# Kernel optimization log

Measured on AMD Instinct MI355X. Metric: run time of the kernel, lower is better.

Reference implementation:

```python
import jax, jax.numpy as jnp
import numpy as np

B, S, EMBED, DK, DV, M = 8, 1024, 1024, 512, 512, 64


def setup_inputs() -> dict:
    key = jax.random.key(0)
    ks = jax.random.split(key, 9)
    query_in = jax.random.normal(ks[0], (B, S, EMBED), dtype=jnp.float32)
    key_in = jax.random.normal(ks[1], (B, S, EMBED), dtype=jnp.float32)
    value_in = jax.random.normal(ks[2], (B, S, EMBED), dtype=jnp.float32)
    lim = 1.0 / np.sqrt(EMBED)  # nn.Linear default init range
    u = lambda k, shape: jax.random.uniform(k, shape, minval=-lim, maxval=lim, dtype=jnp.float32)
    return {
        'query_in': query_in, 'key_in': key_in, 'value_in': value_in,
        'Wq': u(ks[3], (DK, EMBED)), 'bq': u(ks[4], (DK,)),
        'Wk': u(ks[5], (DK, EMBED)), 'bk': u(ks[6], (DK,)),
        'Wv': u(ks[7], (DV, EMBED)), 'bv': u(ks[8], (DV,)),
    }


def _select_landmarks(k_proj, m):
    # Original code runs recursive RLS sampling (random, host-side) over the m
    # segment-rows of key.reshape(B, m, seg, d) and gathers m of them back,
    # then flattens to (B, S, d). We use a deterministic data-dependent
    # selection (rows ranked by squared norm) with identical gather structure.
    Bb, Ss, d = k_proj.shape
    seg = Ss // m
    kr = k_proj.reshape(Bb, m, seg, d)
    scores = jnp.sum(kr * kr, axis=(2, 3))                      # [B, m]
    idx = jnp.argsort(-scores, axis=1)                          # [B, m]
    land = jnp.take_along_axis(kr, idx[:, :, None, None], axis=1)
    return land.reshape(Bb, Ss, d)                              # [B, S, d]


def reference(query_in, key_in, value_in, Wq, bq, Wk, bk, Wv, bv):
    scaling = DK ** -0.25  # 1/sqrt(sqrt(d_k)), applied to both q and k
    q = (jnp.einsum('bse,de->bsd', query_in, Wq) + bq) * scaling
    k = (jnp.einsum('bse,de->bsd', key_in, Wk) + bk) * scaling
    v = jnp.einsum('bse,de->bsd', value_in, Wv) + bv

    kl = _select_landmarks(k, M)                                # [B, S, DK]
    # is_decoder_self_attn is hard-coded True upstream -> q_landmarks = q,
    # so kernel_2 == kernel_1.
    kernel_1 = jax.nn.softmax(jnp.einsum('bqd,bkd->bqk', q, kl), axis=-1)
    kernel_2 = kernel_1
    kernel_3 = jax.nn.softmax(jnp.einsum('bqd,bkd->bqk', q, k), axis=-1)

    k2_inv = jnp.linalg.pinv(kernel_2)                          # [B, S, S] batched SVD
    out = jnp.einsum('bqk,bkd->bqd', jnp.einsum('bqm,bmk->bqk', kernel_1, k2_inv),
                     jnp.einsum('bqk,bkd->bqd', kernel_3, v))
    # dropout is identity in eval mode
    return out
```

## Files before the change

kernel.cpp:

```cpp
#include <hip/hip_runtime.h>
#include <hip/hip_bf16.h>

#define SS   1024
#define DKK  512

typedef __hip_bfloat16 bf16;
typedef __attribute__((ext_vector_type(8))) short s16x8;
typedef __attribute__((ext_vector_type(8))) unsigned short u16x8;
typedef __attribute__((ext_vector_type(4))) float f32x4;

#define WS_W(z)  ((48ull << 20) + ((size_t)(z) << 20))
#define WS_ST    (51ull << 20)
#define WS_Q     (52ull << 20)
#define WS_K     (60ull << 20)
#define WS_VT    (68ull << 20)
#define WS_LG    (0ull)

__device__ __forceinline__ void async_ld16(const void* g, void* s) {
  __builtin_amdgcn_global_load_lds(
      (const __attribute__((address_space(1))) void*)g,
      (__attribute__((address_space(3))) void*)s, 16, 0, 0);
}

__device__ __forceinline__ unsigned short f2bfu(float f) {
  return __builtin_bit_cast(unsigned short, __float2bfloat16(f));
}
__device__ __forceinline__ float bfu2f(unsigned short u) {
  unsigned int i = ((unsigned int)u) << 16;
  return __builtin_bit_cast(float, i);
}

__global__ __launch_bounds__(256)
void convert_w(const float* __restrict__ w0, const float* __restrict__ w1,
               const float* __restrict__ w2, char* __restrict__ ws)
{
  const int bx = blockIdx.x;
  const int z = bx >> 8, local = bx & 255;
  const float* src = (z == 0) ? w0 : (z == 1) ? w1 : w2;
  unsigned short* dst = (unsigned short*)(ws + WS_W(z));
  const int i = local * 2048 + threadIdx.x * 8;
  const float4* s = (const float4*)(src + i);
  float4 a = s[0], b = s[1];
  ushort4 o0, o1;
  o0.x = f2bfu(a.x); o0.y = f2bfu(a.y); o0.z = f2bfu(a.z); o0.w = f2bfu(a.w);
  o1.x = f2bfu(b.x); o1.y = f2bfu(b.y); o1.z = f2bfu(b.z); o1.w = f2bfu(b.w);
  ((ushort4*)(dst + i))[0] = o0;
  ((ushort4*)(dst + i))[1] = o1;
}

template<int BM, int BN, int K, int LDA, int LDB>
__device__ __forceinline__ void gemm_core(const bf16* __restrict__ A,
                                          const bf16* __restrict__ Bw,
                                          int bm, int bn,
                                          short* As, short* Bs, f32x4* acc)
{
  constexpr int MI = BM / 32, NI = BN / 32;
  constexpr int AR = BM / 4,  BR = BN / 4;
  const int tid  = threadIdx.x;
  const int lane = tid & 63;
  const int wave = tid >> 6;
  const int l8   = lane >> 3;
  const int kch  = ((lane & 7) ^ l8) * 8;
  const bf16* ag = A  + (size_t)(bm * BM + wave * AR + l8) * LDA + kch;
  const bf16* bg = Bw + (size_t)(bn * BN + wave * BR + l8) * LDB + kch;
  short* AsW = As + wave * AR * 64;
  short* BsW = Bs + wave * BR * 64;
  const int waveM = wave >> 1, waveN = wave & 1;
  const int l16  = lane & 15;
  const int quad = lane >> 4;
  const int xr   = l16 & 7;

  #pragma unroll
  for (int t = 0; t < MI * NI; ++t)
    #pragma unroll
    for (int r = 0; r < 4; ++r) acc[t][r] = 0.0f;

  for (int kt = 0; kt < K / 64; ++kt) {
    #pragma unroll
    for (int j = 0; j < AR / 8; ++j) async_ld16(ag + (size_t)j * 8 * LDA, AsW + j * 8 * 64);
    #pragma unroll
    for (int j = 0; j < BR / 8; ++j) async_ld16(bg + (size_t)j * 8 * LDB, BsW + j * 8 * 64);
    ag += 64; bg += 64;
    __syncthreads();
    #pragma unroll
    for (int ks = 0; ks < 2; ++ks) {
      s16x8 af[MI], bfv[NI];
      #pragma unroll
      for (int mi = 0; mi < MI; ++mi) {
        const int row  = waveM * (BM / 2) + mi * 16 + l16;
        const int slot = (ks * 4 + quad) ^ xr;
        af[mi] = *(const s16x8*)&As[row * 64 + slot * 8];
      }
      #pragma unroll
      for (int ni = 0; ni < NI; ++ni) {
        const int row  = waveN * (BN / 2) + ni * 16 + l16;
        const int slot = (ks * 4 + quad) ^ xr;
        bfv[ni] = *(const s16x8*)&Bs[row * 64 + slot * 8];
      }
      #pragma unroll
      for (int mi = 0; mi < MI; ++mi)
        #pragma unroll
        for (int ni = 0; ni < NI; ++ni)
          acc[mi * NI + ni] = __builtin_amdgcn_mfma_f32_16x16x32_bf16(
              af[mi], bfv[ni], acc[mi * NI + ni], 0, 0, 0);
    }
    __syncthreads();
  }
}

template<int K, int LDA, int LDB>
__device__ __forceinline__ void gemm_core_f32a(const float* __restrict__ A,
                                               const bf16* __restrict__ Bw,
                                               int bm, int bn,
                                               short* As, short* Bs, f32x4* acc)
{
  const int tid  = threadIdx.x;
  const int lane = tid & 63;
  const int wave = tid >> 6;
  const int l8   = lane >> 3;
  const int kch  = ((lane & 7) ^ l8) * 8;
  const bf16* bg = Bw + (size_t)(bn * 256 + wave * 64 + l8) * LDB + kch;
  short* BsW = Bs + wave * 64 * 64;
  const int arow = tid >> 3;
  const int ag8  = tid & 7;
  const int slotA = (ag8 ^ (arow & 7)) * 8;
  const float* ag = A + (size_t)(bm * 64 + arow) * LDA + ag8 * 8;
  const int waveM = wave >> 1, waveN = wave & 1;
  const int l16  = lane & 15;
  const int quad = lane >> 4;
  const int xr   = l16 & 7;

  #pragma unroll
  for (int t = 0; t < 16; ++t)
    #pragma unroll
    for (int r = 0; r < 4; ++r) acc[t][r] = 0.0f;

  for (int kt = 0; kt < K / 64; ++kt) {
    #pragma unroll
    for (int j = 0; j < 8; ++j) async_ld16(bg + (size_t)j * 8 * LDB, BsW + j * 8 * 64);
    bg += 64;
    #pragma unroll
    for (int p = 0; p < 2; ++p) {
      const float4* s = (const float4*)(ag + (size_t)p * 32 * LDA);
      float4 a = s[0], b = s[1];
      u16x8 v;
      v[0] = f2bfu(a.x); v[1] = f2bfu(a.y); v[2] = f2bfu(a.z); v[3] = f2bfu(a.w);
      v[4] = f2bfu(b.x); v[5] = f2bfu(b.y); v[6] = f2bfu(b.z); v[7] = f2bfu(b.w);
      *(u16x8*)&As[(p * 32 + arow) * 64 + slotA] = v;
    }
    ag += 64;
    __syncthreads();
    #pragma unroll
    for (int ks = 0; ks < 2; ++ks) {
      s16x8 af[2], bfv[8];
      #pragma unroll
      for (int mi = 0; mi < 2; ++mi) {
        const int row  = waveM * 32 + mi * 16 + l16;
        const int slot = (ks * 4 + quad) ^ xr;
        af[mi] = *(const s16x8*)&As[row * 64 + slot * 8];
      }
      #pragma unroll
      for (int ni = 0; ni < 8; ++ni) {
        const int row  = waveN * 128 + ni * 16 + l16;
        const int slot = (ks * 4 + quad) ^ xr;
        bfv[ni] = *(const s16x8*)&Bs[row * 64 + slot * 8];
      }
      #pragma unroll
      for (int mi = 0; mi < 2; ++mi)
        #pragma unroll
        for (int ni = 0; ni < 8; ++ni)
          acc[mi * 8 + ni] = __builtin_amdgcn_mfma_f32_16x16x32_bf16(
              af[mi], bfv[ni], acc[mi * 8 + ni], 0, 0, 0);
    }
    __syncthreads();
  }
}

__global__ __launch_bounds__(256, 3)
void proj_kernel(const float* __restrict__ Xq, const float* __restrict__ Xk,
                 const float* __restrict__ Xv, const bf16* __restrict__ W0,
                 const float* __restrict__ bq, const float* __restrict__ bk,
                 const float* __restrict__ bv,
                 bf16* __restrict__ qo, bf16* __restrict__ ko,
                 bf16* __restrict__ vT, float qscale)
{
  __shared__ __align__(16) short As[64 * 64];
  __shared__ __align__(16) short Bs[256 * 64];
  const int id   = blockIdx.x;
  const int xcd  = id & 7;
  const int s    = id >> 3;
  const int bn   = s & 1;
  const int pair = (s >> 1) * 8 + xcd;
  const int bm   = pair & 127;
  const int z    = pair >> 7;
  const float* A  = (z == 0) ? Xq : (z == 1) ? Xk : Xv;
  const bf16*  Bw = W0 + ((size_t)z << 19);
  const float* bias = (z == 0) ? bq : (z == 1) ? bk : bv;
  f32x4 acc[16];
  gemm_core_f32a<1024, 1024, 1024>(A, Bw, bm, bn, As, Bs, acc);

  const int lane = threadIdx.x & 63;
  const int wave = threadIdx.x >> 6;
  const int waveM = wave >> 1, waveN = wave & 1;
  const int l16 = lane & 15, quad = lane >> 4;
  const int row0 = bm * 64 + waveM * 32;
  const int col0 = bn * 256 + waveN * 128;
  const float sc = (z == 0) ? qscale : 1.0f;
  bf16* C = (z == 0) ? qo : ko;
  #pragma unroll
  for (int ni = 0; ni < 8; ++ni) {
    const int col = col0 + ni * 16 + l16;
    const float bb = bias[col];
    #pragma unroll
    for (int mi = 0; mi < 2; ++mi)
      #pragma unroll
      for (int r = 0; r < 4; ++r) {
        const int row = row0 + mi * 16 + quad * 4 + r;
        const float v = acc[mi * 8 + ni][r] + bb;
        if (z == 2)
          vT[((size_t)(row >> 10) * DKK + col) * SS + (row & (SS - 1))] =
              __float2bfloat16(v);
        else
          C[(size_t)row * DKK + col] = __float2bfloat16(v * sc);
      }
  }
}

__global__ __launch_bounds__(256, 3)
void scores_kernel(const bf16* __restrict__ q, const bf16* __restrict__ k,
                   unsigned short* __restrict__ Pp, float* __restrict__ stats)
{
  __shared__ __align__(16) short As[128 * 64];
  __shared__ __align__(16) short Bs[128 * 64];
  const int z = blockIdx.z;
  const int bn = blockIdx.x, bm = blockIdx.y;
  f32x4 acc[16];
  gemm_core<128, 128, 512, 512, 512>(q + (size_t)z * SS * DKK,
                                     k + (size_t)z * SS * DKK,
                                     bm, bn, As, Bs, acc);

  const int lane = threadIdx.x & 63;
  const int wave = threadIdx.x >> 6;
  const int waveM = wave >> 1, waveN = wave & 1;
  const int l16 = lane & 15, quad = lane >> 4;
  const int row0 = bm * 128 + waveM * 64;
  const int col0 = bn * 128 + waveN * 64;
  const int chunk = bn * 2 + waveN;
  unsigned short* C = Pp + (size_t)z * SS * SS;
  #pragma unroll
  for (int mi = 0; mi < 4; ++mi)
    #pragma unroll
    for (int r = 0; r < 4; ++r) {
      const int row = row0 + mi * 16 + quad * 4 + r;
      float x[4];
      #pragma unroll
      for (int ni = 0; ni < 4; ++ni) x[ni] = acc[mi * 4 + ni][r];
      float m = fmaxf(fmaxf(x[0], x[1]), fmaxf(x[2], x[3]));
      #pragma unroll
      for (int msk = 1; msk < 16; msk <<= 1) m = fmaxf(m, __shfl_xor(m, msk));
      float e[4], ssum = 0.f;
      #pragma unroll
      for (int ni = 0; ni < 4; ++ni) { e[ni] = __expf(x[ni] - m); ssum += e[ni]; }
      #pragma unroll
      for (int msk = 1; msk < 16; msk <<= 1) ssum += __shfl_xor(ssum, msk);
      #pragma unroll
      for (int ni = 0; ni < 4; ++ni)
        C[(size_t)row * SS + col0 + ni * 16 + l16] = f2bfu(e[ni]);
      if (l16 == 0) {
        float2 mr; mr.x = m; mr.y = ssum;
        *(float2*)&stats[(((size_t)z * SS + row) * 16 + chunk) * 2] = mr;
      }
    }
}

__device__ __forceinline__ void gemm_core_pvF(const unsigned short* __restrict__ Pp,
                                              const bf16* __restrict__ vT,
                                              int bm, int bn, const float* Fl,
                                              short* As, short* Bs, f32x4* acc)
{
  const int tid  = threadIdx.x;
  const int lane = tid & 63;
  const int wave = tid >> 6;
  const int l8   = lane >> 3;
  const int kch  = ((lane & 7) ^ l8) * 8;
  const bf16* bg = vT + (size_t)(bn * 64 + wave * 16 + l8) * 1024 + kch;
  short* BsW = Bs + wave * 16 * 64;
  const int arow = tid >> 3;
  const int ag8  = tid & 7;
  const int slotA = (ag8 ^ (arow & 7)) * 8;
  const unsigned short* ag = Pp + (size_t)(bm * 128 + arow) * 1024 + ag8 * 8;
  const int waveM = wave >> 1, waveN = wave & 1;
  const int l16  = lane & 15;
  const int quad = lane >> 4;
  const int xr   = l16 & 7;

  #pragma unroll
  for (int t = 0; t < 8; ++t)
    #pragma unroll
    for (int r = 0; r < 4; ++r) acc[t][r] = 0.0f;

  for (int kt = 0; kt < 16; ++kt) {
    #pragma unroll
    for (int j = 0; j < 2; ++j) async_ld16(bg + (size_t)j * 8 * 1024, BsW + j * 8 * 64);
    bg += 64;
    #pragma unroll
    for (int p = 0; p < 4; ++p) {
      const int rl = p * 32 + arow;
      u16x8 u = *(const u16x8*)(ag + (size_t)p * 32 * 1024);
      const float f = Fl[rl * 17 + kt];
      u16x8 v;
      #pragma unroll
      for (int j = 0; j < 8; ++j)
        v[j] = f2bfu(bfu2f((unsigned short)u[j]) * f);
      *(u16x8*)&As[rl * 64 + slotA] = v;
    }
    ag += 64;
    __syncthreads();
    #pragma unroll
    for (int ks = 0; ks < 2; ++ks) {
      s16x8 af[4], bfv[2];
      #pragma unroll
      for (int mi = 0; mi < 4; ++mi) {
        const int row  = waveM * 64 + mi * 16 + l16;
        const int slot = (ks * 4 + quad) ^ xr;
        af[mi] = *(const s16x8*)&As[row * 64 + slot * 8];
      }
      #pragma unroll
      for (int ni = 0; ni < 2; ++ni) {
        const int row  = waveN * 32 + ni * 16 + l16;
        const int slot = (ks * 4 + quad) ^ xr;
        bfv[ni] = *(const s16x8*)&Bs[row * 64 + slot * 8];
      }
      #pragma unroll
      for (int mi = 0; mi < 4; ++mi)
        #pragma unroll
        for (int ni = 0; ni < 2; ++ni)
          acc[mi * 2 + ni] = __builtin_amdgcn_mfma_f32_16x16x32_bf16(
              af[mi], bfv[ni], acc[mi * 2 + ni], 0, 0, 0);
    }
    __syncthreads();
  }
}

__global__ __launch_bounds__(256, 3)
void pv_kernel(const unsigned short* __restrict__ Pp, const bf16* __restrict__ vT,
               const float* __restrict__ stats, float* __restrict__ out)
{
  __shared__ __align__(16) short As[128 * 64];
  __shared__ __align__(16) short Bs[64 * 64];
  __shared__ float Fl[128 * 17];
  const int z = blockIdx.z;
  const int bn = blockIdx.x, bm = blockIdx.y;
  const int tid = threadIdx.x;

  if (tid < 128) {
    const float* st = stats + ((size_t)z * SS + bm * 128 + tid) * 32;
    float mc[16], lc[16];
    float M = -1e30f;
    #pragma unroll
    for (int c = 0; c < 16; ++c) {
      mc[c] = st[c * 2]; lc[c] = st[c * 2 + 1];
      M = fmaxf(M, mc[c]);
    }
    float L = 0.f;
    #pragma unroll
    for (int c = 0; c < 16; ++c) {
      mc[c] = __expf(mc[c] - M);
      L += mc[c] * lc[c];
    }
    const float R = 1.0f / L;
    #pragma unroll
    for (int c = 0; c < 16; ++c) Fl[tid * 17 + c] = mc[c] * R;
  }
  __syncthreads();

  f32x4 acc[8];
  gemm_core_pvF(Pp + (size_t)z * SS * SS, vT + (size_t)z * DKK * SS,
                bm, bn, Fl, As, Bs, acc);

  const int lane = tid & 63;
  const int wave = tid >> 6;
  const int waveM = wave >> 1, waveN = wave & 1;
  const int l16 = lane & 15, quad = lane >> 4;
  const int row0 = bm * 128 + waveM * 64;
  const int col0 = bn * 64 + waveN * 32;
  float* C = out + (size_t)z * SS * DKK;
  #pragma unroll
  for (int ni = 0; ni < 2; ++ni) {
    const int col = col0 + ni * 16 + l16;
    #pragma unroll
    for (int mi = 0; mi < 4; ++mi)
      #pragma unroll
      for (int r = 0; r < 4; ++r) {
        const int row = row0 + mi * 16 + quad * 4 + r;
        C[(size_t)row * DKK + col] = acc[mi * 2 + ni][r];
      }
  }
}

extern "C" void kernel_launch(void* const* d_in, const int* in_sizes, int n_in,
                              void* d_out, int out_size, void* d_ws, size_t ws_size,
                              hipStream_t stream)
{
  char* ws = (char*)d_ws;
  bf16*  W0   = (bf16*)(ws + WS_W(0));
  float* stat = (float*)(ws + WS_ST);
  bf16*  q    = (bf16*)(ws + WS_Q);
  bf16*  kk   = (bf16*)(ws + WS_K);
  bf16*  vT   = (bf16*)(ws + WS_VT);
  unsigned short* Pp = (unsigned short*)(ws + WS_LG);

  const float qscale = 0.044194173824159216f;

  dim3 blk(256, 1, 1);
  hipLaunchKernelGGL(convert_w, dim3(768), blk, 0, stream,
                     (const float*)d_in[3], (const float*)d_in[5],
                     (const float*)d_in[7], ws);
  hipLaunchKernelGGL(proj_kernel, dim3(768, 1, 1), blk, 0, stream,
                     (const float*)d_in[0], (const float*)d_in[1],
                     (const float*)d_in[2], W0,
                     (const float*)d_in[4], (const float*)d_in[6],
                     (const float*)d_in[8], q, kk, vT, qscale);
  hipLaunchKernelGGL(scores_kernel, dim3(8, 8, 8), blk, 0, stream,
                     q, kk, Pp, stat);
  hipLaunchKernelGGL(pv_kernel, dim3(8, 8, 8), blk, 0, stream,
                     Pp, vT, stat, (float*)d_out);
}
```

Baseline: 221.8 us.

## Retile projection GEMM to 128x128 with async fp32 A staging in LDS

The projection kernel moves from 64x256 tiles to 128x128 tiles on a plain 3D grid, dropping the XCD-aware block remap. The fp32 activation tile is now copied straight into LDS with asynchronous global-to-LDS loads under an XOR swizzle, and the conversion to bf16 happens at fragment-read time instead of through registers before the store. This is meant to cut the register round-trip and the extra A-tile traffic and give a more balanced MFMA tile. In exchange it uses 48KB of LDS per block (fp32 A tile), which may lower occupancy, and each fragment is converted again whenever it is read.

```diff
diff --git a/kernel.cpp b/kernel.cpp
--- a/kernel.cpp
+++ b/kernel.cpp
@@ -108,74 +108,6 @@
   }
 }
 
-template<int K, int LDA, int LDB>
-__device__ __forceinline__ void gemm_core_f32a(const float* __restrict__ A,
-                                               const bf16* __restrict__ Bw,
-                                               int bm, int bn,
-                                               short* As, short* Bs, f32x4* acc)
-{
-  const int tid  = threadIdx.x;
-  const int lane = tid & 63;
-  const int wave = tid >> 6;
-  const int l8   = lane >> 3;
-  const int kch  = ((lane & 7) ^ l8) * 8;
-  const bf16* bg = Bw + (size_t)(bn * 256 + wave * 64 + l8) * LDB + kch;
-  short* BsW = Bs + wave * 64 * 64;
-  const int arow = tid >> 3;
-  const int ag8  = tid & 7;
-  const int slotA = (ag8 ^ (arow & 7)) * 8;
-  const float* ag = A + (size_t)(bm * 64 + arow) * LDA + ag8 * 8;
-  const int waveM = wave >> 1, waveN = wave & 1;
-  const int l16  = lane & 15;
-  const int quad = lane >> 4;
-  const int xr   = l16 & 7;
-
-  #pragma unroll
-  for (int t = 0; t < 16; ++t)
-    #pragma unroll
-    for (int r = 0; r < 4; ++r) acc[t][r] = 0.0f;
-
-  for (int kt = 0; kt < K / 64; ++kt) {
-    #pragma unroll
-    for (int j = 0; j < 8; ++j) async_ld16(bg + (size_t)j * 8 * LDB, BsW + j * 8 * 64);
-    bg += 64;
-    #pragma unroll
-    for (int p = 0; p < 2; ++p) {
-      const float4* s = (const float4*)(ag + (size_t)p * 32 * LDA);
-      float4 a = s[0], b = s[1];
-      u16x8 v;
-      v[0] = f2bfu(a.x); v[1] = f2bfu(a.y); v[2] = f2bfu(a.z); v[3] = f2bfu(a.w);
-      v[4] = f2bfu(b.x); v[5] = f2bfu(b.y); v[6] = f2bfu(b.z); v[7] = f2bfu(b.w);
-      *(u16x8*)&As[(p * 32 + arow) * 64 + slotA] = v;
-    }
-    ag += 64;
-    __syncthreads();
-    #pragma unroll
-    for (int ks = 0; ks < 2; ++ks) {
-      s16x8 af[2], bfv[8];
-      #pragma unroll
-      for (int mi = 0; mi < 2; ++mi) {
-        const int row  = waveM * 32 + mi * 16 + l16;
-        const int slot = (ks * 4 + quad) ^ xr;
-        af[mi] = *(const s16x8*)&As[row * 64 + slot * 8];
-      }
-      #pragma unroll
-      for (int ni = 0; ni < 8; ++ni) {
-        const int row  = waveN * 128 + ni * 16 + l16;
-        const int slot = (ks * 4 + quad) ^ xr;
-        bfv[ni] = *(const s16x8*)&Bs[row * 64 + slot * 8];
-      }
-      #pragma unroll
-      for (int mi = 0; mi < 2; ++mi)
-        #pragma unroll
-        for (int ni = 0; ni < 8; ++ni)
-          acc[mi * 8 + ni] = __builtin_amdgcn_mfma_f32_16x16x32_bf16(
-              af[mi], bfv[ni], acc[mi * 8 + ni], 0, 0, 0);
-    }
-    __syncthreads();
-  }
-}
-
 __global__ __launch_bounds__(256, 3)
 void proj_kernel(const float* __restrict__ Xq, const float* __restrict__ Xk,
                  const float* __restrict__ Xv, const bf16* __restrict__ W0,
@@ -184,39 +116,94 @@
                  bf16* __restrict__ qo, bf16* __restrict__ ko,
                  bf16* __restrict__ vT, float qscale)
 {
-  __shared__ __align__(16) short As[64 * 64];
-  __shared__ __align__(16) short Bs[256 * 64];
-  const int id   = blockIdx.x;
-  const int xcd  = id & 7;
-  const int s    = id >> 3;
-  const int bn   = s & 1;
-  const int pair = (s >> 1) * 8 + xcd;
-  const int bm   = pair & 127;
-  const int z    = pair >> 7;
+  __shared__ __align__(16) float Asf[128 * 64];
+  __shared__ __align__(16) short Bs[128 * 64];
+  const int z  = blockIdx.z;
+  const int bm = blockIdx.x, bn = blockIdx.y;
   const float* A  = (z == 0) ? Xq : (z == 1) ? Xk : Xv;
   const bf16*  Bw = W0 + ((size_t)z << 19);
   const float* bias = (z == 0) ? bq : (z == 1) ? bk : bv;
+
+  const int tid  = threadIdx.x;
+  const int lane = tid & 63;
+  const int wave = tid >> 6;
+  const int l8   = lane >> 3;
+  const int kchB = ((lane & 7) ^ l8) * 8;
+  const bf16* bg = Bw + (size_t)(bn * 128 + wave * 32 + l8) * 1024 + kchB;
+  short* BsW = Bs + wave * 32 * 64;
+  const int arow4 = lane >> 4;
+  const int aslot = lane & 15;
+  const float* ag_row = A + (size_t)(bm * 128 + wave * 32 + arow4) * 1024;
+  float* AsfW = Asf + (wave * 32) * 64;
+
+  const int waveM = wave >> 1, waveN = wave & 1;
+  const int l16  = lane & 15;
+  const int quad = lane >> 4;
+
   f32x4 acc[16];
-  gemm_core_f32a<1024, 1024, 1024>(A, Bw, bm, bn, As, Bs, acc);
-
-  const int lane = threadIdx.x & 63;
-  const int wave = threadIdx.x >> 6;
-  const int waveM = wave >> 1, waveN = wave & 1;
-  const int l16 = lane & 15, quad = lane >> 4;
-  const int row0 = bm * 64 + waveM * 32;
-  const int col0 = bn * 256 + waveN * 128;
+  #pragma unroll
+  for (int t = 0; t < 16; ++t)
+    #pragma unroll
+    for (int r = 0; r < 4; ++r) acc[t][r] = 0.0f;
+
+  for (int kt = 0; kt < 16; ++kt) {
+    #pragma unroll
+    for (int j = 0; j < 8; ++j) {
+      const int gch = aslot ^ ((j * 4 + arow4) & 15);
+      async_ld16(ag_row + (size_t)j * 4 * 1024 + kt * 64 + gch * 4,
+                 AsfW + j * 4 * 64);
+    }
+    #pragma unroll
+    for (int j = 0; j < 4; ++j)
+      async_ld16(bg + (size_t)j * 8 * 1024, BsW + j * 8 * 64);
+    bg += 64;
+    __syncthreads();
+    #pragma unroll
+    for (int ks = 0; ks < 2; ++ks) {
+      s16x8 af[4], bfv[4];
+      #pragma unroll
+      for (int mi = 0; mi < 4; ++mi) {
+        const int row = waveM * 64 + mi * 16 + l16;
+        const int c0  = ks * 8 + quad * 2;
+        const f32x4 a0 = *(const f32x4*)&Asf[row * 64 + ((c0 ^ l16) * 4)];
+        const f32x4 a1 = *(const f32x4*)&Asf[row * 64 + (((c0 + 1) ^ l16) * 4)];
+        u16x8 v;
+        v[0] = f2bfu(a0[0]); v[1] = f2bfu(a0[1]);
+        v[2] = f2bfu(a0[2]); v[3] = f2bfu(a0[3]);
+        v[4] = f2bfu(a1[0]); v[5] = f2bfu(a1[1]);
+        v[6] = f2bfu(a1[2]); v[7] = f2bfu(a1[3]);
+        af[mi] = __builtin_bit_cast(s16x8, v);
+      }
+      #pragma unroll
+      for (int ni = 0; ni < 4; ++ni) {
+        const int row  = waveN * 64 + ni * 16 + l16;
+        const int slot = (ks * 4 + quad) ^ (l16 & 7);
+        bfv[ni] = *(const s16x8*)&Bs[row * 64 + slot * 8];
+      }
+      #pragma unroll
+      for (int mi = 0; mi < 4; ++mi)
+        #pragma unroll
+        for (int ni = 0; ni < 4; ++ni)
+          acc[mi * 4 + ni] = __builtin_amdgcn_mfma_f32_16x16x32_bf16(
+              af[mi], bfv[ni], acc[mi * 4 + ni], 0, 0, 0);
+    }
+    __syncthreads();
+  }
+
+  const int row0 = bm * 128 + waveM * 64;
+  const int col0 = bn * 128 + waveN * 64;
   const float sc = (z == 0) ? qscale : 1.0f;
   bf16* C = (z == 0) ? qo : ko;
   #pragma unroll
-  for (int ni = 0; ni < 8; ++ni) {
+  for (int ni = 0; ni < 4; ++ni) {
     const int col = col0 + ni * 16 + l16;
     const float bb = bias[col];
     #pragma unroll
-    for (int mi = 0; mi < 2; ++mi)
+    for (int mi = 0; mi < 4; ++mi)
       #pragma unroll
       for (int r = 0; r < 4; ++r) {
         const int row = row0 + mi * 16 + quad * 4 + r;
-        const float v = acc[mi * 8 + ni][r] + bb;
+        const float v = acc[mi * 4 + ni][r] + bb;
         if (z == 2)
           vT[((size_t)(row >> 10) * DKK + col) * SS + (row & (SS - 1))] =
               __float2bfloat16(v);
@@ -416,7 +403,7 @@
   hipLaunchKernelGGL(convert_w, dim3(768), blk, 0, stream,
                      (const float*)d_in[3], (const float*)d_in[5],
                      (const float*)d_in[7], ws);
-  hipLaunchKernelGGL(proj_kernel, dim3(768, 1, 1), blk, 0, stream,
+  hipLaunchKernelGGL(proj_kernel, dim3(64, 4, 3), blk, 0, stream,
                      (const float*)d_in[0], (const float*)d_in[1],
                      (const float*)d_in[2], W0,
                      (const float*)d_in[4], (const float*)d_in[6],
```

Result: slower. 229.8 us (+3.6%).
